# Optimization experiments

Measured on AMD Instinct MI355X. Metric: run time of the kernel, lower is better.

## Reference

```python
import jax, jax.numpy as jnp
import numpy as np

N = 50000      # num nodes
E0 = 400000    # raw directed edges
F = 64         # latent_dim (in and per-head out)
H = 2          # num_heads
L = 2          # num_layers
NEG_SLOPE = 0.2


def _build_edges(src_raw, dst_raw):
    # dgl.to_bidirected(dgl.graph((src,dst))) then add_self_loop
    s = np.asarray(src_raw, dtype=np.int64)
    d = np.asarray(dst_raw, dtype=np.int64)
    s2 = np.concatenate([s, d])
    d2 = np.concatenate([d, s])
    code = np.unique(s2 * N + d2)                      # dedupe (bidirected simple graph)
    s2, d2 = code // N, code % N
    keep = s2 != d2                                    # drop existing self loops
    s2, d2 = s2[keep], d2[keep]
    loops = np.arange(N, dtype=np.int64)
    s2 = np.concatenate([s2, loops])
    d2 = np.concatenate([d2, loops])
    return jnp.asarray(s2, jnp.int32), jnp.asarray(d2, jnp.int32)


def setup_inputs() -> dict:
    key = jax.random.key(0)
    kh, ks, kd, kw1, kb1, kw2, kb2, ka = jax.random.split(key, 8)
    src_raw = jax.random.randint(ks, (E0,), 0, N, dtype=jnp.int32)
    dst_raw = jax.random.randint(kd, (E0,), 0, N, dtype=jnp.int32)
    src, dst = _build_edges(np.asarray(src_raw), np.asarray(dst_raw))
    h = jax.random.normal(kh, (N, F), dtype=jnp.float32)
    scale = 1.0 / np.sqrt(F)
    Wsrc = jax.random.normal(kw1, (L, F, H * F), dtype=jnp.float32) * scale
    bsrc = jnp.zeros((L, H * F), dtype=jnp.float32)
    Wdst = jax.random.normal(kw2, (L, F, H * F), dtype=jnp.float32) * scale
    bdst = jnp.zeros((L, H * F), dtype=jnp.float32)
    attn = jax.random.normal(ka, (L, H, F), dtype=jnp.float32) * scale
    return {"h": h, "Wsrc": Wsrc, "bsrc": bsrc, "Wdst": Wdst, "bdst": bdst,
            "attn": attn, "src": src, "dst": dst}


def _gatv2_layer(h, Wsrc, bsrc, Wdst, bdst, attn, src, dst):
    # h: [N,F] -> per-head projections [N,H,F]
    fs = (h @ Wsrc + bsrc).reshape(N, H, F)
    fd = (h @ Wdst + bdst).reshape(N, H, F)
    # per-edge GATv2 logits: a^T leaky_relu(W_s h_u + W_d h_v)
    e = jax.nn.leaky_relu(fs[src] + fd[dst], NEG_SLOPE)      # [E,H,F]
    logits = jnp.einsum("ehf,hf->eh", e, attn)               # [E,H]
    # edge-softmax over incoming edges of each dst node
    m = jax.ops.segment_max(logits, dst, num_segments=N)     # [N,H]
    ex = jnp.exp(logits - m[dst])
    denom = jax.ops.segment_sum(ex, dst, num_segments=N)     # [N,H]
    alpha = ex / denom[dst]                                  # [E,H]
    # scatter-weighted aggregation
    out = jax.ops.segment_sum(alpha[:, :, None] * fs[src], dst, num_segments=N)  # [N,H,F]
    return out.mean(axis=1)                                  # head mean -> [N,F]


def reference(h, Wsrc, bsrc, Wdst, bdst, attn, src, dst):
    for l in range(L):
        h = _gatv2_layer(h, Wsrc[l], bsrc[l], Wdst[l], bdst[l], attn[l], src, dst)
    return h
```

## Files before the change

kernel.cpp:

```cpp
#include <hip/hip_runtime.h>


#define RLN2 1.4426950408889634f

typedef _Float16 half4v __attribute__((ext_vector_type(4)));
typedef _Float16 half2v __attribute__((ext_vector_type(2)));

template <int CTRL>
__device__ __forceinline__ float dpp_add(float x) {
  return x + __int_as_float(__builtin_amdgcn_update_dpp(
                 0, __float_as_int(x), CTRL, 0xF, 0xF, true));
}

__device__ __forceinline__ float xor16_add(float x) {
  return x + __int_as_float(
                 __builtin_amdgcn_ds_swizzle(__float_as_int(x), 0x401F));
}

__device__ __forceinline__ float dot2(half2v a, half2v b, float c) {
#if __has_builtin(__builtin_amdgcn_fdot2)
  return __builtin_amdgcn_fdot2(a, b, c, false);
#else
  return fmaf((float)a.x, (float)b.x, fmaf((float)a.y, (float)b.y, c));
#endif
}

__device__ __forceinline__ half2v lo2(half4v v) {
  return __builtin_shufflevector(v, v, 0, 1);
}
__device__ __forceinline__ half2v hi2(half4v v) {
  return __builtin_shufflevector(v, v, 2, 3);
}

__global__ void rowstart_kernel(const int* __restrict__ src,
                                int* __restrict__ row_start, int EM, int n) {
  int v = blockIdx.x * blockDim.x + threadIdx.x;
  if (v > n) return;
  if (v == n) { row_start[n] = EM; return; }
  int lo = 0, hi = EM;
  while (lo < hi) {
    int mid = (lo + hi) >> 1;
    if (src[mid] < v) lo = mid + 1; else hi = mid;
  }
  row_start[v] = lo;
}

__global__ __launch_bounds__(512) void proj2_kernel(
    const float* __restrict__ hin, const float* __restrict__ Ws,
    const float* __restrict__ bs, const float* __restrict__ Wd,
    const float* __restrict__ bd, _Float16* __restrict__ fs16,
    _Float16* __restrict__ fd16, int n) {
  __shared__ float lds[12544];
  int tid = threadIdx.x;
  int tile = blockIdx.x >> 1;
  int half = blockIdx.x & 1;
  int fb = half * 32;
  int row0 = tile * 64;

  const float4* Ws4 = (const float4*)Ws;
  const float4* Wd4 = (const float4*)Wd;
#pragma unroll
  for (int t = 0; t < 2; ++t) {
    int g = tid + t * 512;
    int k = g >> 4, part = (g >> 3) & 1, c4 = g & 7;
    int srcf4 = k * 32 + part * 16 + half * 8 + c4;
    float4 vs = Ws4[srcf4];
    float4 vd = Wd4[srcf4];
    int base = k * 64 + 8 * c4 + part;
    lds[base + 0] = vs.x; lds[base + 2] = vs.y;
    lds[base + 4] = vs.z; lds[base + 6] = vs.w;
    lds[4096 + base + 0] = vd.x; lds[4096 + base + 2] = vd.y;
    lds[4096 + base + 4] = vd.z; lds[4096 + base + 6] = vd.w;
  }
  const float4* h4 = (const float4*)hin;
#pragma unroll
  for (int t = 0; t < 2; ++t) {
    int idx = tid + t * 512;
    int r = idx >> 4, c = idx & 15;
    int rr = min(row0 + r, n - 1);
    *(float4*)&lds[8192 + r * 68 + c * 4] = h4[(size_t)rr * 16 + c];
  }
  __syncthreads();

  const float* WsL = lds;
  const float* WdL = lds + 4096;
  const float* hL = lds + 8192;

  int jh = tid & 15;
  int rg = tid >> 4;
  int r0 = rg * 2;

  float4 as0 = make_float4(0, 0, 0, 0), as1 = make_float4(0, 0, 0, 0);
  float4 ad0 = make_float4(0, 0, 0, 0), ad1 = make_float4(0, 0, 0, 0);

#pragma unroll 4
  for (int k4 = 0; k4 < 16; ++k4) {
    float4 hv0 = *(const float4*)&hL[r0 * 68 + k4 * 4];
    float4 hv1 = *(const float4*)&hL[(r0 + 1) * 68 + k4 * 4];
    float h0a[4] = {hv0.x, hv0.y, hv0.z, hv0.w};
    float h1a[4] = {hv1.x, hv1.y, hv1.z, hv1.w};
#pragma unroll
    for (int kk = 0; kk < 4; ++kk) {
      int k = k4 * 4 + kk;
      float4 ws = *(const float4*)&WsL[k * 64 + jh * 4];
      float4 wd = *(const float4*)&WdL[k * 64 + jh * 4];
      as0.x = fmaf(h0a[kk], ws.x, as0.x); as0.y = fmaf(h0a[kk], ws.y, as0.y);
      as0.z = fmaf(h0a[kk], ws.z, as0.z); as0.w = fmaf(h0a[kk], ws.w, as0.w);
      as1.x = fmaf(h1a[kk], ws.x, as1.x); as1.y = fmaf(h1a[kk], ws.y, as1.y);
      as1.z = fmaf(h1a[kk], ws.z, as1.z); as1.w = fmaf(h1a[kk], ws.w, as1.w);
      ad0.x = fmaf(h0a[kk], wd.x, ad0.x); ad0.y = fmaf(h0a[kk], wd.y, ad0.y);
      ad0.z = fmaf(h0a[kk], wd.z, ad0.z); ad0.w = fmaf(h0a[kk], wd.w, ad0.w);
      ad1.x = fmaf(h1a[kk], wd.x, ad1.x); ad1.y = fmaf(h1a[kk], wd.y, ad1.y);
      ad1.z = fmaf(h1a[kk], wd.z, ad1.z); ad1.w = fmaf(h1a[kk], wd.w, ad1.w);
    }
  }

  int j0 = fb + 2 * jh, j1 = j0 + 1;
  float4 bsv = make_float4(bs[j0], bs[64 + j0], bs[j1], bs[64 + j1]);
  float4 bdv = make_float4(bd[j0], bd[64 + j0], bd[j1], bd[64 + j1]);
#pragma unroll
  for (int r = 0; r < 2; ++r) {
    int rr = row0 + r0 + r;
    if (rr < n) {
      float4 a = r ? as1 : as0;
      float4 d = r ? ad1 : ad0;
      half2v s_h0 = {(_Float16)(a.x + bsv.x), (_Float16)(a.z + bsv.z)};
      half2v s_h1 = {(_Float16)(a.y + bsv.y), (_Float16)(a.w + bsv.w)};
      half2v d_h0 = {(_Float16)(d.x + bdv.x), (_Float16)(d.z + bdv.z)};
      half2v d_h1 = {(_Float16)(d.y + bdv.y), (_Float16)(d.w + bdv.w)};
      *(half2v*)&fs16[(size_t)rr * 128 + j0] = s_h0;
      *(half2v*)&fs16[(size_t)rr * 128 + 64 + j0] = s_h1;
      *(half2v*)&fd16[(size_t)rr * 128 + j0] = d_h0;
      *(half2v*)&fd16[(size_t)rr * 128 + 64 + j0] = d_h1;
    }
  }
}

#define EDGE_LOGIT(x0, x1, p0, p1)                                      \
  {                                                                     \
    half4v t0 = (x0) + fdh0;                                            \
    half4v t1 = (x1) + fdh1;                                            \
    half4v m0 = __builtin_elementwise_max(t0, t0 * c02);                \
    half4v m1 = __builtin_elementwise_max(t1, t1 * c02);                \
    p0 = dot2(hi2(m0), a0hi, dot2(lo2(m0), a0lo, 0.f));                 \
    p1 = dot2(hi2(m1), a1hi, dot2(lo2(m1), a1lo, 0.f));                 \
    p0 = dpp_add<0xB1>(p0);  p1 = dpp_add<0xB1>(p1);                    \
    p0 = dpp_add<0x4E>(p0);  p1 = dpp_add<0x4E>(p1);                    \
    p0 = dpp_add<0x141>(p0); p1 = dpp_add<0x141>(p1);                   \
    p0 = dpp_add<0x140>(p0); p1 = dpp_add<0x140>(p1);                   \
  }

#define EDGE_ACC(x0, x1, w0, w1)                                        \
  {                                                                     \
    d0 += (w0); d1 += (w1);                                             \
    acc0.x = fmaf((w0), (float)(x0).x, acc0.x);                         \
    acc0.y = fmaf((w0), (float)(x0).y, acc0.y);                         \
    acc0.z = fmaf((w0), (float)(x0).z, acc0.z);                         \
    acc0.w = fmaf((w0), (float)(x0).w, acc0.w);                         \
    acc1.x = fmaf((w1), (float)(x1).x, acc1.x);                         \
    acc1.y = fmaf((w1), (float)(x1).y, acc1.y);                         \
    acc1.z = fmaf((w1), (float)(x1).z, acc1.z);                         \
    acc1.w = fmaf((w1), (float)(x1).w, acc1.w);                         \
  }

__global__ __launch_bounds__(256) void gat_node_kernel(
    const _Float16* __restrict__ fs16, const _Float16* __restrict__ fd16,
    const float* __restrict__ attn, const int* __restrict__ row_start,
    const int* __restrict__ nbr, float* __restrict__ out, int n) {
  int wid = (int)((blockIdx.x * 256 + threadIdx.x) >> 6);
  int lane = threadIdx.x & 63;
  if (wid >= n) return;
  int lp = lane & 15;
  int slot = lane >> 4;

  half2v a0lo = {(_Float16)(attn[4 * lp] * RLN2),
                 (_Float16)(attn[4 * lp + 1] * RLN2)};
  half2v a0hi = {(_Float16)(attn[4 * lp + 2] * RLN2),
                 (_Float16)(attn[4 * lp + 3] * RLN2)};
  half2v a1lo = {(_Float16)(attn[64 + 4 * lp] * RLN2),
                 (_Float16)(attn[64 + 4 * lp + 1] * RLN2)};
  half2v a1hi = {(_Float16)(attn[64 + 4 * lp + 2] * RLN2),
                 (_Float16)(attn[64 + 4 * lp + 3] * RLN2)};
  const half4v c02 = {(_Float16)0.2f, (_Float16)0.2f, (_Float16)0.2f,
                      (_Float16)0.2f};

  const half4v* fsH = (const half4v*)fs16;
  const half4v* fdH = (const half4v*)fd16;
  half4v fdh0 = fdH[(size_t)wid * 32 + lp];
  half4v fdh1 = fdH[(size_t)wid * 32 + 16 + lp];

  float4 acc0 = make_float4(0, 0, 0, 0), acc1 = make_float4(0, 0, 0, 0);
  float d0 = 0.f, d1 = 0.f;

  {
    half4v x0 = fsH[(size_t)wid * 32 + lp];
    half4v x1 = fsH[(size_t)wid * 32 + 16 + lp];
    float p0, p1;
    EDGE_LOGIT(x0, x1, p0, p1);
    float w0 = __builtin_amdgcn_exp2f(p0);
    float w1 = __builtin_amdgcn_exp2f(p1);
    if (slot != 0) { w0 = 0.f; w1 = 0.f; }
    EDGE_ACC(x0, x1, w0, w1);
  }

  int e0 = row_start[wid], e1 = row_start[wid + 1];
  if (e0 < e1) {
    int last = e1 - 1;
    int u0 = nbr[min(e0 + slot, last)];
    half4v xa = fsH[(size_t)u0 * 32 + lp];
    half4v xb = fsH[(size_t)u0 * 32 + 16 + lp];
    int uN = nbr[min(e0 + 4 + slot, last)];

    for (int i = e0; i < e1; i += 4) {
      int uNN = nbr[min(i + 8 + slot, last)];
      half4v na = fsH[(size_t)uN * 32 + lp];
      half4v nb = fsH[(size_t)uN * 32 + 16 + lp];

      float p0, p1;
      EDGE_LOGIT(xa, xb, p0, p1);
      float w0 = __builtin_amdgcn_exp2f(p0);
      float w1 = __builtin_amdgcn_exp2f(p1);
      if (i + slot >= e1) { w0 = 0.f; w1 = 0.f; }
      EDGE_ACC(xa, xb, w0, w1);

      xa = na; xb = nb; uN = uNN;
    }
  }

  acc0.x = xor16_add(acc0.x); acc0.y = xor16_add(acc0.y);
  acc0.z = xor16_add(acc0.z); acc0.w = xor16_add(acc0.w);
  acc1.x = xor16_add(acc1.x); acc1.y = xor16_add(acc1.y);
  acc1.z = xor16_add(acc1.z); acc1.w = xor16_add(acc1.w);
  d0 = xor16_add(d0); d1 = xor16_add(d1);
  acc0.x += __shfl_xor(acc0.x, 32, 64); acc0.y += __shfl_xor(acc0.y, 32, 64);
  acc0.z += __shfl_xor(acc0.z, 32, 64); acc0.w += __shfl_xor(acc0.w, 32, 64);
  acc1.x += __shfl_xor(acc1.x, 32, 64); acc1.y += __shfl_xor(acc1.y, 32, 64);
  acc1.z += __shfl_xor(acc1.z, 32, 64); acc1.w += __shfl_xor(acc1.w, 32, 64);
  d0 += __shfl_xor(d0, 32, 64); d1 += __shfl_xor(d1, 32, 64);

  if (lane < 16) {
    float rd0 = 1.0f / d0, rd1 = 1.0f / d1;
    float4 o;
    o.x = 0.5f * (acc0.x * rd0 + acc1.x * rd1);
    o.y = 0.5f * (acc0.y * rd0 + acc1.y * rd1);
    o.z = 0.5f * (acc0.z * rd0 + acc1.z * rd1);
    o.w = 0.5f * (acc0.w * rd0 + acc1.w * rd1);
    ((float4*)out)[(size_t)wid * 16 + lp] = o;
  }
}

extern "C" void kernel_launch(void* const* d_in, const int* in_sizes, int n_in,
                              void* d_out, int out_size, void* d_ws, size_t ws_size,
                              hipStream_t stream) {
  const float* h    = (const float*)d_in[0];
  const float* Wsrc = (const float*)d_in[1];
  const float* bsrc = (const float*)d_in[2];
  const float* Wdst = (const float*)d_in[3];
  const float* bdst = (const float*)d_in[4];
  const float* attn = (const float*)d_in[5];
  const int*   src  = (const int*)d_in[6];
  const int*   dst  = (const int*)d_in[7];
  int E = in_sizes[6];
  int N = in_sizes[0] / 64;
  int EM = E - N;
  float* out = (float*)d_out;

  _Float16* fs16      = (_Float16*)d_ws;
  _Float16* fd16      = fs16 + (size_t)N * 128;
  int*      row_start = (int*)(fd16 + (size_t)N * 128);

  rowstart_kernel<<<(N + 256) / 256, 256, 0, stream>>>(src, row_start, EM, N);

  int pb = ((N + 63) / 64) * 2;
  int nb = (N + 3) / 4;
  for (int l = 0; l < 2; ++l) {
    const float* hin = (l == 0) ? h : out;
    proj2_kernel<<<pb, 512, 0, stream>>>(hin, Wsrc + (size_t)l * 64 * 128,
                                         bsrc + (size_t)l * 128,
                                         Wdst + (size_t)l * 64 * 128,
                                         bdst + (size_t)l * 128, fs16, fd16, N);
    gat_node_kernel<<<nb, 256, 0, stream>>>(fs16, fd16, attn + (size_t)l * 128,
                                            row_start, dst, out, N);
  }
}
```

Before: 161.5 us.

## Interleave head features into 16-byte chunks and deepen gather prefetch

The projection kernel now stores fs/fd so that each lane's four features for head 0 and head 1 sit next to each other in one 16-byte chunk. The aggregation kernel can then fetch both heads with a single half8 load instead of two half4 loads. The edge loop is unrolled by two with a three-deep prefetch of neighbour rows, adding memory-level parallelism to the random gathers. The cost is more live registers and a more complex tail path for the last one or two edge groups.

```diff
diff --git a/kernel.cpp b/kernel.cpp
--- a/kernel.cpp
+++ b/kernel.cpp
@@ -3,7 +3,7 @@
 
 #define RLN2 1.4426950408889634f
 
-typedef _Float16 half4v __attribute__((ext_vector_type(4)));
+typedef _Float16 half8v __attribute__((ext_vector_type(8)));
 typedef _Float16 half2v __attribute__((ext_vector_type(2)));
 
 template <int CTRL>
@@ -23,13 +23,6 @@
 #else
   return fmaf((float)a.x, (float)b.x, fmaf((float)a.y, (float)b.y, c));
 #endif
-}
-
-__device__ __forceinline__ half2v lo2(half4v v) {
-  return __builtin_shufflevector(v, v, 0, 1);
-}
-__device__ __forceinline__ half2v hi2(half4v v) {
-  return __builtin_shufflevector(v, v, 2, 3);
 }
 
 __global__ void rowstart_kernel(const int* __restrict__ src,
@@ -118,6 +111,8 @@
   int j0 = fb + 2 * jh, j1 = j0 + 1;
   float4 bsv = make_float4(bs[j0], bs[64 + j0], bs[j1], bs[64 + j1]);
   float4 bdv = make_float4(bd[j0], bd[64 + j0], bd[j1], bd[64 + j1]);
+  int c0 = j0 >> 2, o = j0 & 3;
+  int base = c0 * 8 + o;
 #pragma unroll
   for (int r = 0; r < 2; ++r) {
     int rr = row0 + r0 + r;
@@ -128,40 +123,13 @@
       half2v s_h1 = {(_Float16)(a.y + bsv.y), (_Float16)(a.w + bsv.w)};
       half2v d_h0 = {(_Float16)(d.x + bdv.x), (_Float16)(d.z + bdv.z)};
       half2v d_h1 = {(_Float16)(d.y + bdv.y), (_Float16)(d.w + bdv.w)};
-      *(half2v*)&fs16[(size_t)rr * 128 + j0] = s_h0;
-      *(half2v*)&fs16[(size_t)rr * 128 + 64 + j0] = s_h1;
-      *(half2v*)&fd16[(size_t)rr * 128 + j0] = d_h0;
-      *(half2v*)&fd16[(size_t)rr * 128 + 64 + j0] = d_h1;
-    }
-  }
-}
-
-#define EDGE_LOGIT(x0, x1, p0, p1)                                      \
-  {                                                                     \
-    half4v t0 = (x0) + fdh0;                                            \
-    half4v t1 = (x1) + fdh1;                                            \
-    half4v m0 = __builtin_elementwise_max(t0, t0 * c02);                \
-    half4v m1 = __builtin_elementwise_max(t1, t1 * c02);                \
-    p0 = dot2(hi2(m0), a0hi, dot2(lo2(m0), a0lo, 0.f));                 \
-    p1 = dot2(hi2(m1), a1hi, dot2(lo2(m1), a1lo, 0.f));                 \
-    p0 = dpp_add<0xB1>(p0);  p1 = dpp_add<0xB1>(p1);                    \
-    p0 = dpp_add<0x4E>(p0);  p1 = dpp_add<0x4E>(p1);                    \
-    p0 = dpp_add<0x141>(p0); p1 = dpp_add<0x141>(p1);                   \
-    p0 = dpp_add<0x140>(p0); p1 = dpp_add<0x140>(p1);                   \
-  }
-
-#define EDGE_ACC(x0, x1, w0, w1)                                        \
-  {                                                                     \
-    d0 += (w0); d1 += (w1);                                             \
-    acc0.x = fmaf((w0), (float)(x0).x, acc0.x);                         \
-    acc0.y = fmaf((w0), (float)(x0).y, acc0.y);                         \
-    acc0.z = fmaf((w0), (float)(x0).z, acc0.z);                         \
-    acc0.w = fmaf((w0), (float)(x0).w, acc0.w);                         \
-    acc1.x = fmaf((w1), (float)(x1).x, acc1.x);                         \
-    acc1.y = fmaf((w1), (float)(x1).y, acc1.y);                         \
-    acc1.z = fmaf((w1), (float)(x1).z, acc1.z);                         \
-    acc1.w = fmaf((w1), (float)(x1).w, acc1.w);                         \
-  }
+      *(half2v*)&fs16[(size_t)rr * 128 + base] = s_h0;
+      *(half2v*)&fs16[(size_t)rr * 128 + base + 4] = s_h1;
+      *(half2v*)&fd16[(size_t)rr * 128 + base] = d_h0;
+      *(half2v*)&fd16[(size_t)rr * 128 + base + 4] = d_h1;
+    }
+  }
+}
 
 __global__ __launch_bounds__(256) void gat_node_kernel(
     const _Float16* __restrict__ fs16, const _Float16* __restrict__ fd16,
@@ -181,49 +149,72 @@
                  (_Float16)(attn[64 + 4 * lp + 1] * RLN2)};
   half2v a1hi = {(_Float16)(attn[64 + 4 * lp + 2] * RLN2),
                  (_Float16)(attn[64 + 4 * lp + 3] * RLN2)};
-  const half4v c02 = {(_Float16)0.2f, (_Float16)0.2f, (_Float16)0.2f,
-                      (_Float16)0.2f};
-
-  const half4v* fsH = (const half4v*)fs16;
-  const half4v* fdH = (const half4v*)fd16;
-  half4v fdh0 = fdH[(size_t)wid * 32 + lp];
-  half4v fdh1 = fdH[(size_t)wid * 32 + 16 + lp];
+  const half8v c02 = {(_Float16)0.2f, (_Float16)0.2f, (_Float16)0.2f,
+                      (_Float16)0.2f, (_Float16)0.2f, (_Float16)0.2f,
+                      (_Float16)0.2f, (_Float16)0.2f};
+
+  const half8v* fsC = (const half8v*)fs16;
+  const half8v* fdC = (const half8v*)fd16;
+  half8v fdh = fdC[(size_t)wid * 16 + lp];
 
   float4 acc0 = make_float4(0, 0, 0, 0), acc1 = make_float4(0, 0, 0, 0);
   float d0 = 0.f, d1 = 0.f;
 
+#define EDGE_COMPUTE(xv, kill_cond)                                        \
+  {                                                                        \
+    half8v t = (xv) + fdh;                                                 \
+    half8v m = __builtin_elementwise_max(t, t * c02);                      \
+    float p0 = dot2(__builtin_shufflevector(m, m, 0, 1), a0lo, 0.f);       \
+    p0 = dot2(__builtin_shufflevector(m, m, 2, 3), a0hi, p0);              \
+    float p1 = dot2(__builtin_shufflevector(m, m, 4, 5), a1lo, 0.f);       \
+    p1 = dot2(__builtin_shufflevector(m, m, 6, 7), a1hi, p1);              \
+    p0 = dpp_add<0xB1>(p0);  p1 = dpp_add<0xB1>(p1);                       \
+    p0 = dpp_add<0x4E>(p0);  p1 = dpp_add<0x4E>(p1);                       \
+    p0 = dpp_add<0x141>(p0); p1 = dpp_add<0x141>(p1);                      \
+    p0 = dpp_add<0x140>(p0); p1 = dpp_add<0x140>(p1);                      \
+    float w0 = __builtin_amdgcn_exp2f(p0);                                 \
+    float w1 = __builtin_amdgcn_exp2f(p1);                                 \
+    if (kill_cond) { w0 = 0.f; w1 = 0.f; }                                 \
+    d0 += w0; d1 += w1;                                                    \
+    acc0.x = fmaf(w0, (float)(xv)[0], acc0.x);                             \
+    acc0.y = fmaf(w0, (float)(xv)[1], acc0.y);                             \
+    acc0.z = fmaf(w0, (float)(xv)[2], acc0.z);                             \
+    acc0.w = fmaf(w0, (float)(xv)[3], acc0.w);                             \
+    acc1.x = fmaf(w1, (float)(xv)[4], acc1.x);                             \
+    acc1.y = fmaf(w1, (float)(xv)[5], acc1.y);                             \
+    acc1.z = fmaf(w1, (float)(xv)[6], acc1.z);                             \
+    acc1.w = fmaf(w1, (float)(xv)[7], acc1.w);                             \
+  }
+
   {
-    half4v x0 = fsH[(size_t)wid * 32 + lp];
-    half4v x1 = fsH[(size_t)wid * 32 + 16 + lp];
-    float p0, p1;
-    EDGE_LOGIT(x0, x1, p0, p1);
-    float w0 = __builtin_amdgcn_exp2f(p0);
-    float w1 = __builtin_amdgcn_exp2f(p1);
-    if (slot != 0) { w0 = 0.f; w1 = 0.f; }
-    EDGE_ACC(x0, x1, w0, w1);
+    half8v xs = fsC[(size_t)wid * 16 + lp];
+    EDGE_COMPUTE(xs, (slot != 0));
   }
 
   int e0 = row_start[wid], e1 = row_start[wid + 1];
   if (e0 < e1) {
     int last = e1 - 1;
     int u0 = nbr[min(e0 + slot, last)];
-    half4v xa = fsH[(size_t)u0 * 32 + lp];
-    half4v xb = fsH[(size_t)u0 * 32 + 16 + lp];
-    int uN = nbr[min(e0 + 4 + slot, last)];
-
-    for (int i = e0; i < e1; i += 4) {
-      int uNN = nbr[min(i + 8 + slot, last)];
-      half4v na = fsH[(size_t)uN * 32 + lp];
-      half4v nb = fsH[(size_t)uN * 32 + 16 + lp];
-
-      float p0, p1;
-      EDGE_LOGIT(xa, xb, p0, p1);
-      float w0 = __builtin_amdgcn_exp2f(p0);
-      float w1 = __builtin_amdgcn_exp2f(p1);
-      if (i + slot >= e1) { w0 = 0.f; w1 = 0.f; }
-      EDGE_ACC(xa, xb, w0, w1);
-
-      xa = na; xb = nb; uN = uNN;
+    int u1 = nbr[min(e0 + 4 + slot, last)];
+    int u2 = nbr[min(e0 + 8 + slot, last)];
+    half8v x0 = fsC[(size_t)u0 * 16 + lp];
+    half8v x1 = fsC[(size_t)u1 * 16 + lp];
+    half8v x2 = fsC[(size_t)u2 * 16 + lp];
+
+    int i = e0;
+    for (; i + 8 <= e1; i += 8) {
+      int ua = nbr[min(i + 12 + slot, last)];
+      int ub = nbr[min(i + 16 + slot, last)];
+      half8v xa = fsC[(size_t)ua * 16 + lp];
+      EDGE_COMPUTE(x0, (i + slot >= e1));
+      half8v xb = fsC[(size_t)ub * 16 + lp];
+      EDGE_COMPUTE(x1, (i + 4 + slot >= e1));
+      x0 = x2; x1 = xa; x2 = xb;
+    }
+    if (i < e1) {
+      EDGE_COMPUTE(x0, (i + slot >= e1));
+      i += 4;
+      if (i < e1) EDGE_COMPUTE(x1, (i + slot >= e1));
     }
   }
 
@@ -247,6 +238,7 @@
     o.w = 0.5f * (acc0.w * rd0 + acc1.w * rd1);
     ((float4*)out)[(size_t)wid * 16 + lp] = o;
   }
+#undef EDGE_COMPUTE
 }
 
 extern "C" void kernel_launch(void* const* d_in, const int* in_sizes, int n_in,
```

Measured after the change: 156.4 us. 3.2% less time.
